# Optimization experiments

Measured on AMD Instinct MI355X. Metric: run time of the kernel, lower is better.

## Reference

```python
import jax, jax.numpy as jnp
import numpy as np
import math

N_NODES = 50000
N_EDGES = 800000
IN_CH = 128
HID_CH = 16   # per-head channels of conv1
OUT_CH = 1    # per-head channels of conv2 (forced so Linear(heads,100) type-checks)
HEADS = 8


def _seg_softmax(scores, seg, n):
    # softmax over edges grouped by target node (variable-size neighborhoods)
    m = jax.ops.segment_max(scores, seg, num_segments=n)
    e = jnp.exp(scores - m[seg])
    s = jax.ops.segment_sum(e, seg, num_segments=n)
    return e / (s[seg] + 1e-16)


def _transformer_conv(x, edge_index, Wq, bq, Wk, bk, Wv, bv, Ws, bs, heads, ch):
    # PyG TransformerConv, concat=True, root_weight=True, beta=False
    n = x.shape[0]
    src, dst = edge_index[0], edge_index[1]
    q = (x @ Wq + bq).reshape(n, heads, ch)
    k = (x @ Wk + bk).reshape(n, heads, ch)
    v = (x @ Wv + bv).reshape(n, heads, ch)
    qi = q[dst]              # [E, H, C] gather at target
    kj = k[src]              # [E, H, C] gather at source
    vj = v[src]              # [E, H, C]
    alpha = jnp.einsum('ehc,ehc->eh', qi, kj) / math.sqrt(ch)  # [E, H]
    alpha = _seg_softmax(alpha, dst, n)
    agg = jax.ops.segment_sum(vj * alpha[:, :, None], dst, num_segments=n)
    out = agg.reshape(n, heads * ch)
    return out + x @ Ws + bs   # skip connection lin_skip(x)


def setup_inputs() -> dict:
    key = jax.random.key(0)
    ks = jax.random.split(key, 16)
    s = 0.05
    d1 = HEADS * HID_CH  # 128
    d2 = HEADS * OUT_CH  # 8
    inp = {
        'x': jax.random.normal(ks[0], (N_NODES, IN_CH), dtype=jnp.float32),
        'edge_index': jax.random.randint(ks[1], (2, N_EDGES), 0, N_NODES),
        # conv1 params
        'Wq1': jax.random.normal(ks[2], (IN_CH, d1), dtype=jnp.float32) * s,
        'bq1': jnp.zeros((d1,), jnp.float32),
        'Wk1': jax.random.normal(ks[3], (IN_CH, d1), dtype=jnp.float32) * s,
        'bk1': jnp.zeros((d1,), jnp.float32),
        'Wv1': jax.random.normal(ks[4], (IN_CH, d1), dtype=jnp.float32) * s,
        'bv1': jnp.zeros((d1,), jnp.float32),
        'Ws1': jax.random.normal(ks[5], (IN_CH, d1), dtype=jnp.float32) * s,
        'bs1': jnp.zeros((d1,), jnp.float32),
        # conv2 params (in = hidden*heads = 128)
        'Wq2': jax.random.normal(ks[6], (d1, d2), dtype=jnp.float32) * s,
        'bq2': jnp.zeros((d2,), jnp.float32),
        'Wk2': jax.random.normal(ks[7], (d1, d2), dtype=jnp.float32) * s,
        'bk2': jnp.zeros((d2,), jnp.float32),
        'Wv2': jax.random.normal(ks[8], (d1, d2), dtype=jnp.float32) * s,
        'bv2': jnp.zeros((d2,), jnp.float32),
        'Ws2': jax.random.normal(ks[9], (d1, d2), dtype=jnp.float32) * s,
        'bs2': jnp.zeros((d2,), jnp.float32),
        # final linear: heads -> 100
        'Wl': jax.random.normal(ks[10], (HEADS, 100), dtype=jnp.float32) * s,
        'bl': jnp.zeros((100,), jnp.float32),
    }
    return inp


def reference(x, edge_index, Wq1, bq1, Wk1, bk1, Wv1, bv1, Ws1, bs1,
              Wq2, bq2, Wk2, bk2, Wv2, bv2, Ws2, bs2, Wl, bl):
    h = _transformer_conv(x, edge_index, Wq1, bq1, Wk1, bk1, Wv1, bv1, Ws1, bs1, HEADS, HID_CH)
    h = _transformer_conv(h, edge_index, Wq2, bq2, Wk2, bk2, Wv2, bv2, Ws2, bs2, HEADS, OUT_CH)
    h = jax.nn.relu(h @ Wl + bl)   # dropout is identity in eval mode
    return jnp.mean(h, axis=0, keepdims=True)   # [1, 100]
```

## Files before the change

### kernel.cpp

```cpp
#include <hip/hip_runtime.h>
#include <hip/hip_bf16.h>
#include <cstdint>
#include <cstddef>


typedef _Float16 f16x8 __attribute__((ext_vector_type(8)));
typedef _Float16 f16x4 __attribute__((ext_vector_type(4)));
typedef _Float16 f16x2 __attribute__((ext_vector_type(2)));
typedef float    f32x4 __attribute__((ext_vector_type(4)));

__global__ __launch_bounds__(256) void to_half(
    const float* __restrict__ x, _Float16* __restrict__ xh, int total8)
{
    int i = blockIdx.x * 256 + threadIdx.x;
    if (i >= total8) return;
    float4 f0 = ((const float4*)x)[2 * i];
    float4 f1 = ((const float4*)x)[2 * i + 1];
    f16x8 h = { (_Float16)f0.x, (_Float16)f0.y, (_Float16)f0.z, (_Float16)f0.w,
                (_Float16)f1.x, (_Float16)f1.y, (_Float16)f1.z, (_Float16)f1.w };
    ((f16x8*)xh)[i] = h;
}

__global__ __launch_bounds__(256) void pack_weights(
    const float* __restrict__ Wq1, const float* __restrict__ bq1,
    const float* __restrict__ Wk1, const float* __restrict__ bk1,
    const float* __restrict__ Wv1, const float* __restrict__ bv1,
    const float* __restrict__ Ws1, const float* __restrict__ bs1,
    const float* __restrict__ Wq2, const float* __restrict__ bq2,
    const float* __restrict__ Wk2, const float* __restrict__ bk2,
    const float* __restrict__ Wv2, const float* __restrict__ bv2,
    const float* __restrict__ Ws2, const float* __restrict__ bs2,
    _Float16* __restrict__ Wt1, float* __restrict__ b1,
    _Float16* __restrict__ Wt2, float* __restrict__ b2)
{
    int i = blockIdx.x * 256 + threadIdx.x;
    if (i < 65536) {
        int j = i >> 7, k = i & 127;
        const float* W; int col;
        if (j < 128)      { W = Wq1; col = j; }
        else if (j < 384) { int t = j - 128, c = t >> 2, r = t & 3;
                            if (r < 2) { W = Wk1; col = 2 * c + r; }
                            else       { W = Wv1; col = 2 * c + r - 2; } }
        else              { W = Ws1; col = j - 384; }
        Wt1[i] = (_Float16)W[k * 128 + col];
    } else if (i < 66048) {
        int j = i - 65536;
        const float* B; int col;
        if (j < 128)      { B = bq1; col = j; }
        else if (j < 384) { int t = j - 128, c = t >> 2, r = t & 3;
                            if (r < 2) { B = bk1; col = 2 * c + r; }
                            else       { B = bv1; col = 2 * c + r - 2; } }
        else              { B = bs1; col = j - 384; }
        b1[j] = B[col];
    } else if (i < 66048 + 4096) {
        int t = i - 66048;
        int j = t >> 7, k = t & 127;
        const float* W; int col;
        if (j < 8)       { W = Wq2; col = j; }
        else if (j < 24) { int u = j - 8; col = u >> 1; W = (u & 1) ? Wv2 : Wk2; }
        else             { W = Ws2; col = j - 24; }
        Wt2[t] = (_Float16)W[k * 8 + col];
    } else if (i < 66048 + 4096 + 32) {
        int j = i - (66048 + 4096);
        const float* B; int col;
        if (j < 8)       { B = bq2; col = j; }
        else if (j < 24) { int u = j - 8; col = u >> 1; B = (u & 1) ? bv2 : bk2; }
        else             { B = bs2; col = j - 24; }
        b2[j] = B[col];
    }
}

__global__ __launch_bounds__(256) void gemm1(
    const _Float16* __restrict__ xh, const _Float16* __restrict__ Wt1,
    const float* __restrict__ b1, _Float16* __restrict__ qs,
    _Float16* __restrict__ kvbuf, int n)
{
    __shared__ _Float16 As[64][136];
    __shared__ _Float16 Bs[64][136];
    __shared__ _Float16 Ds[64][72];
    int tid = threadIdx.x;
    int colbase = blockIdx.x * 64, rowbase = blockIdx.y * 64;
    #pragma unroll
    for (int it = 0; it < 4; ++it) {
        int c = it * 256 + tid, row = c >> 4, ch = c & 15;
        f16x8 v = {};
        if (rowbase + row < n) v = *(const f16x8*)&xh[(size_t)(rowbase + row) * 128 + ch * 8];
        *(f16x8*)&As[row][ch * 8] = v;
    }
    #pragma unroll
    for (int it = 0; it < 4; ++it) {
        int c = it * 256 + tid, row = c >> 4, ch = c & 15;
        *(f16x8*)&Bs[row][ch * 8] = *(const f16x8*)&Wt1[(size_t)(colbase + row) * 128 + ch * 8];
    }
    __syncthreads();
    int w = tid >> 6, l = tid & 63;
    int wm = w >> 1, wn = w & 1, fr = l & 15, fg = l >> 4;
    f32x4 acc[2][2] = {};
    #pragma unroll
    for (int kk = 0; kk < 4; ++kk) {
        int ko = kk * 32 + fg * 8;
        f16x8 a0 = *(const f16x8*)&As[wm * 32 + fr][ko];
        f16x8 a1 = *(const f16x8*)&As[wm * 32 + 16 + fr][ko];
        f16x8 b0 = *(const f16x8*)&Bs[wn * 32 + fr][ko];
        f16x8 b1v = *(const f16x8*)&Bs[wn * 32 + 16 + fr][ko];
        acc[0][0] = __builtin_amdgcn_mfma_f32_16x16x32_f16(a0, b0, acc[0][0], 0, 0, 0);
        acc[0][1] = __builtin_amdgcn_mfma_f32_16x16x32_f16(a0, b1v, acc[0][1], 0, 0, 0);
        acc[1][0] = __builtin_amdgcn_mfma_f32_16x16x32_f16(a1, b0, acc[1][0], 0, 0, 0);
        acc[1][1] = __builtin_amdgcn_mfma_f32_16x16x32_f16(a1, b1v, acc[1][1], 0, 0, 0);
    }
    #pragma unroll
    for (int nt = 0; nt < 2; ++nt) {
        int col = wn * 32 + nt * 16 + fr;
        float bv = b1[colbase + col];
        #pragma unroll
        for (int mt = 0; mt < 2; ++mt)
            #pragma unroll
            for (int r = 0; r < 4; ++r)
                Ds[wm * 32 + mt * 16 + fg * 4 + r][col] = (_Float16)(acc[mt][nt][r] + bv);
    }
    __syncthreads();
    _Float16* dst; int dcol;
    if (colbase < 128)      { dst = qs;    dcol = colbase; }
    else if (colbase < 384) { dst = kvbuf; dcol = colbase - 128; }
    else                    { dst = qs;    dcol = colbase - 256; }
    #pragma unroll
    for (int it = 0; it < 2; ++it) {
        int c = it * 256 + tid, row = c >> 3, ch = c & 7;
        if (rowbase + row < n)
            *(f16x8*)&dst[(size_t)(rowbase + row) * 256 + dcol + ch * 8] =
                *(const f16x8*)&Ds[row][ch * 8];
    }
}

__global__ __launch_bounds__(256) void count_edges(
    const int* __restrict__ ei, int* __restrict__ counts, int E)
{
    int e = blockIdx.x * 256 + threadIdx.x;
    if (e < E) atomicAdd(&counts[ei[E + e]], 1);
}

__global__ __launch_bounds__(256) void scan1(
    const int* __restrict__ counts, int* __restrict__ indptr,
    int* __restrict__ blocksums, int n)
{
    int t = threadIdx.x, b = blockIdx.x, i = b * 256 + t;
    int v = (i < n) ? counts[i] : 0;
    int x = v;
    #pragma unroll
    for (int off = 1; off < 64; off <<= 1) {
        int y = __shfl_up(x, off, 64);
        if ((t & 63) >= off) x += y;
    }
    __shared__ int wsum[4];
    if ((t & 63) == 63) wsum[t >> 6] = x;
    __syncthreads();
    int woff = 0;
    for (int w = 0; w < (t >> 6); ++w) woff += wsum[w];
    if (i < n) indptr[i] = woff + x - v;
    if (t == 255) blocksums[b] = woff + x;
}

__global__ __launch_bounds__(256) void scan2(
    const int* __restrict__ blocksums, int* __restrict__ blockoff,
    int* __restrict__ indptr, int nb, int n, int E)
{
    int t = threadIdx.x;
    int v = (t < nb) ? blocksums[t] : 0;
    int x = v;
    #pragma unroll
    for (int off = 1; off < 64; off <<= 1) {
        int y = __shfl_up(x, off, 64);
        if ((t & 63) >= off) x += y;
    }
    __shared__ int wsum[4];
    if ((t & 63) == 63) wsum[t >> 6] = x;
    __syncthreads();
    int woff = 0;
    for (int w = 0; w < (t >> 6); ++w) woff += wsum[w];
    if (t < nb) blockoff[t] = woff + x - v;
    if (t == 0) indptr[n] = E;
}

__global__ __launch_bounds__(256) void scan3(
    int* __restrict__ indptr, const int* __restrict__ blockoff, int n)
{
    int i = blockIdx.x * 256 + threadIdx.x;
    if (i < n) indptr[i] += blockoff[blockIdx.x];
}

__global__ __launch_bounds__(256) void scatter_edges(
    const int* __restrict__ ei, const int* __restrict__ indptr,
    int* __restrict__ fill, int* __restrict__ srcs, int E)
{
    int e = blockIdx.x * 256 + threadIdx.x;
    if (e < E) {
        int d = ei[E + e];
        int pos = indptr[d] + atomicAdd(&fill[d], 1);
        srcs[pos] = ei[e];
    }
}

__global__ __launch_bounds__(256) void attn1(
    const _Float16* __restrict__ qs, const _Float16* __restrict__ kvbuf,
    const int* __restrict__ indptr, const int* __restrict__ srcs,
    _Float16* __restrict__ h1, int n)
{
    int wid = threadIdx.x >> 6, l = threadIdx.x & 63;
    int node = blockIdx.x * 4 + wid;
    if (node >= n) return;
    const _Float16* nrow = qs + (size_t)node * 256;
    f16x2 qh = ((const f16x2*)nrow)[l];
    float q0 = (float)qh.x * 0.25f, q1 = (float)qh.y * 0.25f;
    float den = 0.f, a0 = 0.f, a1 = 0.f;

    auto edge = [&](f16x4 kv) {
        float p = fmaf(q0, (float)kv.x, q1 * (float)kv.y);
        p += __shfl_xor(p, 1, 64);
        p += __shfl_xor(p, 2, 64);
        p += __shfl_xor(p, 4, 64);
        float w = __expf(p);
        den += w;
        a0 = fmaf(w, (float)kv.z, a0);
        a1 = fmaf(w, (float)kv.w, a1);
    };

    int i0 = indptr[node], deg = indptr[node + 1] - i0;
    for (int base = 0; base < deg; base += 64) {
        int cnt = min(64, deg - base);
        int sv = (base + l < deg) ? srcs[i0 + base + l] : 0;
        int e = 0;
        for (; e + 4 <= cnt; e += 4) {
            int s0 = __builtin_amdgcn_readfirstlane(__shfl(sv, e));
            int s1 = __builtin_amdgcn_readfirstlane(__shfl(sv, e + 1));
            int s2 = __builtin_amdgcn_readfirstlane(__shfl(sv, e + 2));
            int s3 = __builtin_amdgcn_readfirstlane(__shfl(sv, e + 3));
            f16x4 kv0 = ((const f16x4*)(kvbuf + (size_t)s0 * 256))[l];
            f16x4 kv1 = ((const f16x4*)(kvbuf + (size_t)s1 * 256))[l];
            f16x4 kv2 = ((const f16x4*)(kvbuf + (size_t)s2 * 256))[l];
            f16x4 kv3 = ((const f16x4*)(kvbuf + (size_t)s3 * 256))[l];
            edge(kv0); edge(kv1); edge(kv2); edge(kv3);
        }
        for (; e < cnt; ++e) {
            int s0 = __builtin_amdgcn_readfirstlane(__shfl(sv, e));
            f16x4 kv = ((const f16x4*)(kvbuf + (size_t)s0 * 256))[l];
            edge(kv);
        }
    }
    float inv = 1.f / (den + 1e-16f);
    f16x2 s2v = ((const f16x2*)(nrow + 128))[l];
    f16x2 o;
    o.x = (_Float16)(a0 * inv + (float)s2v.x);
    o.y = (_Float16)(a1 * inv + (float)s2v.y);
    ((f16x2*)(h1 + (size_t)node * 128))[l] = o;
}

__global__ __launch_bounds__(256) void gemm2(
    const _Float16* __restrict__ h1, const _Float16* __restrict__ Wt2,
    const float* __restrict__ b2, _Float16* __restrict__ qkvs2, int n)
{
    __shared__ _Float16 As[64][136];
    __shared__ _Float16 Bs[32][136];
    int tid = threadIdx.x;
    int rowbase = blockIdx.x * 64;
    #pragma unroll
    for (int it = 0; it < 4; ++it) {
        int c = it * 256 + tid, row = c >> 4, ch = c & 15;
        f16x8 v = {};
        if (rowbase + row < n) v = *(const f16x8*)&h1[(size_t)(rowbase + row) * 128 + ch * 8];
        *(f16x8*)&As[row][ch * 8] = v;
    }
    #pragma unroll
    for (int it = 0; it < 2; ++it) {
        int c = it * 256 + tid, row = c >> 4, ch = c & 15;
        *(f16x8*)&Bs[row][ch * 8] = *(const f16x8*)&Wt2[row * 128 + ch * 8];
    }
    __syncthreads();
    int w = tid >> 6, l = tid & 63, fr = l & 15, fg = l >> 4;
    f32x4 acc[2] = {};
    #pragma unroll
    for (int kk = 0; kk < 4; ++kk) {
        int ko = kk * 32 + fg * 8;
        f16x8 a = *(const f16x8*)&As[w * 16 + fr][ko];
        f16x8 b0 = *(const f16x8*)&Bs[fr][ko];
        f16x8 b1v = *(const f16x8*)&Bs[16 + fr][ko];
        acc[0] = __builtin_amdgcn_mfma_f32_16x16x32_f16(a, b0, acc[0], 0, 0, 0);
        acc[1] = __builtin_amdgcn_mfma_f32_16x16x32_f16(a, b1v, acc[1], 0, 0, 0);
    }
    #pragma unroll
    for (int nt = 0; nt < 2; ++nt) {
        int col = nt * 16 + fr;
        float bv = b2[col];
        #pragma unroll
        for (int r = 0; r < 4; ++r) {
            int row = rowbase + w * 16 + fg * 4 + r;
            if (row < n) qkvs2[(size_t)row * 32 + col] = (_Float16)(acc[nt][r] + bv);
        }
    }
}

__global__ __launch_bounds__(256) void attn2(
    const _Float16* __restrict__ q2, const int* __restrict__ indptr,
    const int* __restrict__ srcs, float* __restrict__ h2, int n)
{
    int wid = threadIdx.x >> 6, l = threadIdx.x & 63;
    int node = blockIdx.x * 4 + wid;
    if (node >= n) return;
    int i = l >> 3, h = l & 7;
    const _Float16* base = q2 + (size_t)node * 32;
    float qh = (float)base[h];
    int i0 = indptr[node], i1 = indptr[node + 1];
    float den = 0.f, acc = 0.f;
    for (int p = i0 + i; p < i1; p += 8) {
        int s = srcs[p];
        f16x2 kv = ((const f16x2*)(q2 + (size_t)s * 32 + 8))[h];
        float w = __expf(qh * (float)kv.x);
        den += w;
        acc = fmaf(w, (float)kv.y, acc);
    }
    den += __shfl_xor(den, 8, 64); den += __shfl_xor(den, 16, 64); den += __shfl_xor(den, 32, 64);
    acc += __shfl_xor(acc, 8, 64); acc += __shfl_xor(acc, 16, 64); acc += __shfl_xor(acc, 32, 64);
    if (i == 0)
        h2[(size_t)node * 8 + h] = acc / (den + 1e-16f) + (float)base[24 + h];
}

__global__ __launch_bounds__(128) void final_reduce(
    const float* __restrict__ h2, const float* __restrict__ Wl,
    const float* __restrict__ bl, float* __restrict__ out, int n, int chunk)
{
    int j = threadIdx.x;
    bool act = j < 100;
    float wl[8] = {};
    float bj = 0.f;
    if (act) {
        #pragma unroll
        for (int t = 0; t < 8; ++t) wl[t] = Wl[t * 100 + j];
        bj = bl[j];
    }
    int lo = blockIdx.x * chunk, hi = min(n, lo + chunk);
    float acc = 0.f;
    for (int node = lo; node < hi; ++node) {
        const float* hr = h2 + (size_t)node * 8;
        float y = bj;
        #pragma unroll
        for (int t = 0; t < 8; ++t) y += hr[t] * wl[t];
        acc += fmaxf(y, 0.f);
    }
    if (act) atomicAdd(&out[j], acc * (1.f / (float)n));
}

extern "C" void kernel_launch(void* const* d_in, const int* in_sizes, int n_in,
                              void* d_out, int out_size, void* d_ws, size_t ws_size,
                              hipStream_t stream)
{
    const float* x   = (const float*)d_in[0];
    const int*   ei  = (const int*)d_in[1];
    const float* Wq1 = (const float*)d_in[2],  *bq1 = (const float*)d_in[3];
    const float* Wk1 = (const float*)d_in[4],  *bk1 = (const float*)d_in[5];
    const float* Wv1 = (const float*)d_in[6],  *bv1 = (const float*)d_in[7];
    const float* Ws1 = (const float*)d_in[8],  *bs1 = (const float*)d_in[9];
    const float* Wq2 = (const float*)d_in[10], *bq2 = (const float*)d_in[11];
    const float* Wk2 = (const float*)d_in[12], *bk2 = (const float*)d_in[13];
    const float* Wv2 = (const float*)d_in[14], *bv2 = (const float*)d_in[15];
    const float* Ws2 = (const float*)d_in[16], *bs2 = (const float*)d_in[17];
    const float* Wl  = (const float*)d_in[18], *bl  = (const float*)d_in[19];
    float* out = (float*)d_out;

    int n = in_sizes[0] / 128;
    int E = in_sizes[1] / 2;

    char* p = (char*)d_ws;
    auto take = [&](size_t bytes) -> void* {
        void* r = (void*)p;
        p += (bytes + 255) & ~(size_t)255;
        return r;
    };
    _Float16* xh     = (_Float16*)take((size_t)n * 128 * 2);
    _Float16* qs     = (_Float16*)take((size_t)n * 256 * 2);
    _Float16* kvbuf  = (_Float16*)take((size_t)n * 256 * 2);
    _Float16* h1     = (_Float16*)take((size_t)n * 128 * 2);
    _Float16* qkvs2  = (_Float16*)take((size_t)n * 32 * 2);
    float*    h2     = (float*)take((size_t)n * 8 * 4);
    _Float16* Wt1    = (_Float16*)take(65536 * 2);
    float*    b1     = (float*)take(512 * 4);
    _Float16* Wt2    = (_Float16*)take(4096 * 2);
    float*    b2     = (float*)take(32 * 4);
    int*      counts = (int*)take((size_t)n * 4);
    int*      fill   = (int*)take((size_t)n * 4);
    int*      indptr = (int*)take((size_t)(n + 1) * 4);
    int*      srcs   = (int*)take((size_t)E * 4);
    int       nb     = (n + 255) / 256;
    int*      blocksums = (int*)take((size_t)nb * 4);
    int*      blockoff  = (int*)take((size_t)nb * 4);

    hipMemsetAsync(counts, 0, (size_t)n * 4, stream);
    hipMemsetAsync(fill, 0, (size_t)n * 4, stream);
    hipMemsetAsync(out, 0, (size_t)out_size * 4, stream);

    to_half<<<(n * 128 / 8 + 255) / 256, 256, 0, stream>>>(x, xh, n * 128 / 8);
    pack_weights<<<(70176 + 255) / 256, 256, 0, stream>>>(
        Wq1, bq1, Wk1, bk1, Wv1, bv1, Ws1, bs1,
        Wq2, bq2, Wk2, bk2, Wv2, bv2, Ws2, bs2,
        Wt1, b1, Wt2, b2);

    count_edges<<<(E + 255) / 256, 256, 0, stream>>>(ei, counts, E);
    scan1<<<nb, 256, 0, stream>>>(counts, indptr, blocksums, n);
    scan2<<<1, 256, 0, stream>>>(blocksums, blockoff, indptr, nb, n, E);
    scan3<<<nb, 256, 0, stream>>>(indptr, blockoff, n);
    scatter_edges<<<(E + 255) / 256, 256, 0, stream>>>(ei, indptr, fill, srcs, E);

    gemm1<<<dim3(8, (n + 63) / 64), 256, 0, stream>>>(xh, Wt1, b1, qs, kvbuf, n);
    attn1<<<(n + 3) / 4, 256, 0, stream>>>(qs, kvbuf, indptr, srcs, h1, n);
    gemm2<<<(n + 63) / 64, 256, 0, stream>>>(h1, Wt2, b2, qkvs2, n);
    attn2<<<(n + 3) / 4, 256, 0, stream>>>(qkvs2, indptr, srcs, h2, n);

    int chunk = (n + 255) / 256;
    final_reduce<<<256, 128, 0, stream>>>(h2, Wl, bl, out, n, chunk);
}
```

Baseline: 345.7 us.

## Fuse fp32-to-half conversion into gemm1 and process two edges per wave in attn1

Removes the separate to_half kernel and its intermediate buffer by having gemm1 load fp32 x directly and convert to half while staging into shared memory. gemm1 has 8 column blocks, so each block now reads the fp32 rows itself, doubling the bytes read per tile while saving one kernel launch and the round trip through xh. attn1 is restructured so each half-wave handles a different edge with 16-byte loads per lane. This halves the shuffle-reduction depth, and a masked tail plus a final cross-half reduction combine the partial sums.

Result: slower. 356.4 us (+3.1%).

```diff
diff --git a/kernel.cpp b/kernel.cpp
--- a/kernel.cpp
+++ b/kernel.cpp
@@ -8,18 +8,6 @@
 typedef _Float16 f16x4 __attribute__((ext_vector_type(4)));
 typedef _Float16 f16x2 __attribute__((ext_vector_type(2)));
 typedef float    f32x4 __attribute__((ext_vector_type(4)));
-
-__global__ __launch_bounds__(256) void to_half(
-    const float* __restrict__ x, _Float16* __restrict__ xh, int total8)
-{
-    int i = blockIdx.x * 256 + threadIdx.x;
-    if (i >= total8) return;
-    float4 f0 = ((const float4*)x)[2 * i];
-    float4 f1 = ((const float4*)x)[2 * i + 1];
-    f16x8 h = { (_Float16)f0.x, (_Float16)f0.y, (_Float16)f0.z, (_Float16)f0.w,
-                (_Float16)f1.x, (_Float16)f1.y, (_Float16)f1.z, (_Float16)f1.w };
-    ((f16x8*)xh)[i] = h;
-}
 
 __global__ __launch_bounds__(256) void pack_weights(
     const float* __restrict__ Wq1, const float* __restrict__ bq1,
@@ -71,7 +59,7 @@
 }
 
 __global__ __launch_bounds__(256) void gemm1(
-    const _Float16* __restrict__ xh, const _Float16* __restrict__ Wt1,
+    const float* __restrict__ x, const _Float16* __restrict__ Wt1,
     const float* __restrict__ b1, _Float16* __restrict__ qs,
     _Float16* __restrict__ kvbuf, int n)
 {
@@ -81,11 +69,12 @@
     int tid = threadIdx.x;
     int colbase = blockIdx.x * 64, rowbase = blockIdx.y * 64;
     #pragma unroll
-    for (int it = 0; it < 4; ++it) {
-        int c = it * 256 + tid, row = c >> 4, ch = c & 15;
-        f16x8 v = {};
-        if (rowbase + row < n) v = *(const f16x8*)&xh[(size_t)(rowbase + row) * 128 + ch * 8];
-        *(f16x8*)&As[row][ch * 8] = v;
+    for (int it = 0; it < 8; ++it) {
+        int c = it * 256 + tid, row = c >> 5, ch = c & 31;
+        float4 v = make_float4(0.f, 0.f, 0.f, 0.f);
+        if (rowbase + row < n) v = *(const float4*)&x[(size_t)(rowbase + row) * 128 + ch * 4];
+        f16x4 hv = { (_Float16)v.x, (_Float16)v.y, (_Float16)v.z, (_Float16)v.w };
+        *(f16x4*)&As[row][ch * 4] = hv;
     }
     #pragma unroll
     for (int it = 0; it < 4; ++it) {
@@ -208,50 +197,67 @@
     int wid = threadIdx.x >> 6, l = threadIdx.x & 63;
     int node = blockIdx.x * 4 + wid;
     if (node >= n) return;
+    int lam = l & 31, half = l >> 5;
     const _Float16* nrow = qs + (size_t)node * 256;
-    f16x2 qh = ((const f16x2*)nrow)[l];
-    float q0 = (float)qh.x * 0.25f, q1 = (float)qh.y * 0.25f;
-    float den = 0.f, a0 = 0.f, a1 = 0.f;
-
-    auto edge = [&](f16x4 kv) {
-        float p = fmaf(q0, (float)kv.x, q1 * (float)kv.y);
+    f16x4 q4 = ((const f16x4*)nrow)[lam];
+    float q0 = (float)q4.x * 0.25f, q1 = (float)q4.y * 0.25f;
+    float q2 = (float)q4.z * 0.25f, q3 = (float)q4.w * 0.25f;
+    float den = 0.f, a0 = 0.f, a1 = 0.f, a2 = 0.f, a3 = 0.f;
+    const char* kvb = (const char*)kvbuf;
+    size_t lane_off = (size_t)(lam * 16);
+
+    auto edge = [&](const f16x8& kv, bool ok) {
+        float p = (float)kv[0] * q0 + (float)kv[1] * q1
+                + (float)kv[4] * q2 + (float)kv[5] * q3;
         p += __shfl_xor(p, 1, 64);
         p += __shfl_xor(p, 2, 64);
-        p += __shfl_xor(p, 4, 64);
-        float w = __expf(p);
+        float w = __expf(ok ? p : -1e30f);
         den += w;
-        a0 = fmaf(w, (float)kv.z, a0);
-        a1 = fmaf(w, (float)kv.w, a1);
+        a0 = fmaf(w, (float)kv[2], a0);
+        a1 = fmaf(w, (float)kv[3], a1);
+        a2 = fmaf(w, (float)kv[6], a2);
+        a3 = fmaf(w, (float)kv[7], a3);
     };
 
     int i0 = indptr[node], deg = indptr[node + 1] - i0;
     for (int base = 0; base < deg; base += 64) {
         int cnt = min(64, deg - base);
-        int sv = (base + l < deg) ? srcs[i0 + base + l] : 0;
+        int sv8 = 0;
+        if (base + l < deg) sv8 = srcs[i0 + base + l] << 9;
         int e = 0;
-        for (; e + 4 <= cnt; e += 4) {
-            int s0 = __builtin_amdgcn_readfirstlane(__shfl(sv, e));
-            int s1 = __builtin_amdgcn_readfirstlane(__shfl(sv, e + 1));
-            int s2 = __builtin_amdgcn_readfirstlane(__shfl(sv, e + 2));
-            int s3 = __builtin_amdgcn_readfirstlane(__shfl(sv, e + 3));
-            f16x4 kv0 = ((const f16x4*)(kvbuf + (size_t)s0 * 256))[l];
-            f16x4 kv1 = ((const f16x4*)(kvbuf + (size_t)s1 * 256))[l];
-            f16x4 kv2 = ((const f16x4*)(kvbuf + (size_t)s2 * 256))[l];
-            f16x4 kv3 = ((const f16x4*)(kvbuf + (size_t)s3 * 256))[l];
-            edge(kv0); edge(kv1); edge(kv2); edge(kv3);
+        for (; e + 8 <= cnt; e += 8) {
+            int oA = __shfl(sv8, e +     half, 64);
+            int oB = __shfl(sv8, e + 2 + half, 64);
+            int oC = __shfl(sv8, e + 4 + half, 64);
+            int oD = __shfl(sv8, e + 6 + half, 64);
+            f16x8 kvA = *(const f16x8*)(kvb + oA + lane_off);
+            f16x8 kvB = *(const f16x8*)(kvb + oB + lane_off);
+            f16x8 kvC = *(const f16x8*)(kvb + oC + lane_off);
+            f16x8 kvD = *(const f16x8*)(kvb + oD + lane_off);
+            edge(kvA, true); edge(kvB, true); edge(kvC, true); edge(kvD, true);
         }
-        for (; e < cnt; ++e) {
-            int s0 = __builtin_amdgcn_readfirstlane(__shfl(sv, e));
-            f16x4 kv = ((const f16x4*)(kvbuf + (size_t)s0 * 256))[l];
-            edge(kv);
+        for (; e < cnt; e += 2) {
+            int idx = e + half;
+            int o = __shfl(sv8, idx, 64);
+            f16x8 kv = *(const f16x8*)(kvb + o + lane_off);
+            edge(kv, idx < cnt);
         }
     }
+    den += __shfl_xor(den, 32, 64);
+    a0 += __shfl_xor(a0, 32, 64);
+    a1 += __shfl_xor(a1, 32, 64);
+    a2 += __shfl_xor(a2, 32, 64);
+    a3 += __shfl_xor(a3, 32, 64);
     float inv = 1.f / (den + 1e-16f);
-    f16x2 s2v = ((const f16x2*)(nrow + 128))[l];
-    f16x2 o;
-    o.x = (_Float16)(a0 * inv + (float)s2v.x);
-    o.y = (_Float16)(a1 * inv + (float)s2v.y);
-    ((f16x2*)(h1 + (size_t)node * 128))[l] = o;
+    f16x4 s4 = ((const f16x4*)(nrow + 128))[lam];
+    if (half == 0) {
+        f16x4 o;
+        o.x = (_Float16)(a0 * inv + (float)s4.x);
+        o.y = (_Float16)(a1 * inv + (float)s4.y);
+        o.z = (_Float16)(a2 * inv + (float)s4.z);
+        o.w = (_Float16)(a3 * inv + (float)s4.w);
+        ((f16x4*)(h1 + (size_t)node * 128))[lam] = o;
+    }
 }
 
 __global__ __launch_bounds__(256) void gemm2(
@@ -374,7 +380,6 @@
         p += (bytes + 255) & ~(size_t)255;
         return r;
     };
-    _Float16* xh     = (_Float16*)take((size_t)n * 128 * 2);
     _Float16* qs     = (_Float16*)take((size_t)n * 256 * 2);
     _Float16* kvbuf  = (_Float16*)take((size_t)n * 256 * 2);
     _Float16* h1     = (_Float16*)take((size_t)n * 128 * 2);
@@ -396,7 +401,6 @@
     hipMemsetAsync(fill, 0, (size_t)n * 4, stream);
     hipMemsetAsync(out, 0, (size_t)out_size * 4, stream);
 
-    to_half<<<(n * 128 / 8 + 255) / 256, 256, 0, stream>>>(x, xh, n * 128 / 8);
     pack_weights<<<(70176 + 255) / 256, 256, 0, stream>>>(
         Wq1, bq1, Wk1, bk1, Wv1, bv1, Ws1, bs1,
         Wq2, bq2, Wk2, bk2, Wv2, bv2, Ws2, bs2,
@@ -408,7 +412,7 @@
     scan3<<<nb, 256, 0, stream>>>(indptr, blockoff, n);
     scatter_edges<<<(E + 255) / 256, 256, 0, stream>>>(ei, indptr, fill, srcs, E);
 
-    gemm1<<<dim3(8, (n + 63) / 64), 256, 0, stream>>>(xh, Wt1, b1, qs, kvbuf, n);
+    gemm1<<<dim3(8, (n + 63) / 64), 256, 0, stream>>>(x, Wt1, b1, qs, kvbuf, n);
     attn1<<<(n + 3) / 4, 256, 0, stream>>>(qs, kvbuf, indptr, srcs, h1, n);
     gemm2<<<(n + 63) / 64, 256, 0, stream>>>(h1, Wt2, b2, qkvs2, n);
     attn2<<<(n + 3) / 4, 256, 0, stream>>>(qkvs2, indptr, srcs, h2, n);
```
